# Performance work log

Hardware: AMD Instinct MI355X
Metric: run time of the kernel (lower is better)

## Reference

```python
import jax, jax.numpy as jnp
import numpy as np

N_NODES = 50000
N_EDGES = 1600000
N_FEAT = 128
HIDDEN = 128
N_GRAPHS = 64
N_CLASSES = 10
N_REGS = 1


def setup_inputs() -> dict:
    key = jax.random.key(0)
    ks = jax.random.split(key, 16)
    inp = {
        "x": jax.random.normal(ks[0], (N_NODES, N_FEAT), dtype=jnp.float32),
        "edge_index": jax.random.randint(ks[1], (2, N_EDGES), 0, N_NODES, dtype=jnp.int32),
        "batch": jnp.sort(jax.random.randint(ks[2], (N_NODES,), 0, N_GRAPHS, dtype=jnp.int32)),
        # GCNConv layer params (PyG: linear without bias applied first, bias added after aggregation)
        "w0": jax.random.normal(ks[3], (N_FEAT, HIDDEN), dtype=jnp.float32) * 0.05,
        "b0": jax.random.normal(ks[4], (HIDDEN,), dtype=jnp.float32) * 0.05,
        "w1": jax.random.normal(ks[5], (HIDDEN, HIDDEN), dtype=jnp.float32) * 0.05,
        "b1": jax.random.normal(ks[6], (HIDDEN,), dtype=jnp.float32) * 0.05,
        "w2": jax.random.normal(ks[7], (HIDDEN, HIDDEN), dtype=jnp.float32) * 0.05,
        "b2": jax.random.normal(ks[8], (HIDDEN,), dtype=jnp.float32) * 0.05,
        # heads
        "wc": jax.random.normal(ks[9], (HIDDEN, N_CLASSES), dtype=jnp.float32) * 0.05,
        "bc": jax.random.normal(ks[10], (N_CLASSES,), dtype=jnp.float32) * 0.05,
        "wr": jax.random.normal(ks[11], (HIDDEN, N_REGS), dtype=jnp.float32) * 0.05,
        "br": jax.random.normal(ks[12], (N_REGS,), dtype=jnp.float32) * 0.05,
    }
    return inp


def _gcn_layer(x, src, dst, w, b, deg_inv_sqrt, deg_inv):
    # x: [N, Din] -> [N, Dout]. GCNConv: D^-1/2 (A+I) D^-1/2 (x W) + b
    h = x @ w  # [N, Dout]
    coef = (deg_inv_sqrt[src] * deg_inv_sqrt[dst])[:, None]  # [E, 1]
    agg = jax.ops.segment_sum(h[src] * coef, dst, num_segments=x.shape[0])
    agg = agg + h * deg_inv[:, None]  # self-loop term: deg^-1 * h
    return agg + b


def reference(x, edge_index, batch, w0, b0, w1, b1, w2, b2, wc, bc, wr, br):
    src, dst = edge_index[0], edge_index[1]
    n = x.shape[0]
    # degrees include self-loop weight 1 (PyG gcn_norm with edge_weight=1)
    deg = jax.ops.segment_sum(jnp.ones(src.shape, x.dtype), dst, num_segments=n) + 1.0
    deg_inv_sqrt = deg ** -0.5
    deg_inv = 1.0 / deg

    h = _gcn_layer(x, src, dst, w0, b0, deg_inv_sqrt, deg_inv)
    h = _gcn_layer(jax.nn.elu(h), src, dst, w1, b1, deg_inv_sqrt, deg_inv)
    h = _gcn_layer(jax.nn.elu(h), src, dst, w2, b2, deg_inv_sqrt, deg_inv)

    # global mean pool over graphs
    sums = jax.ops.segment_sum(h, batch, num_segments=N_GRAPHS)  # [G, H]
    cnt = jax.ops.segment_sum(jnp.ones((n,), h.dtype), batch, num_segments=N_GRAPHS)
    pooled = sums / jnp.maximum(cnt, 1.0)[:, None]

    cls_out = pooled @ wc + bc
    reg_out = pooled @ wr + br
    return (pooled, cls_out, reg_out)
```

## Files before the change

kernel.cpp:

```cpp
#include <hip/hip_runtime.h>
#include <hip/hip_fp16.h>
#include <math.h>

#define N_NODES   50000
#define N_EDGES   1600000
#define NF        128
#define N_GRAPHS  64
#define N_CLASSES 10

#define NBK       391
#define BK_SHIFT  7
#define BK_NODES  128
#define SLAB      5120
#define CHUNK     4096
#define NCHUNKS   ((N_EDGES + CHUNK - 1) / CHUNK)

typedef _Float16 half8 __attribute__((ext_vector_type(8)));
typedef float f32x4 __attribute__((ext_vector_type(4)));

__global__ void k_zero(int* __restrict__ bucket_cur, float* __restrict__ sums) {
    int i = blockIdx.x * 256 + threadIdx.x;
    if (i < NBK) bucket_cur[i] = i * SLAB;
    if (i < N_GRAPHS * NF) sums[i] = 0.f;
}

__global__ __launch_bounds__(256) void k_bscatter(const int* __restrict__ src,
                                                  const int* __restrict__ dst,
                                                  int* __restrict__ bucket_cur,
                                                  int* __restrict__ pairs) {
    __shared__ int h[NBK], rb[NBK], c2[NBK];
    int t = threadIdx.x;
    for (int i = t; i < NBK; i += 256) { h[i] = 0; c2[i] = 0; }
    __syncthreads();
    int base = blockIdx.x * CHUNK;
    int end = min(base + CHUNK, N_EDGES);
    for (int e = base + t; e < end; e += 256)
        atomicAdd(&h[dst[e] >> BK_SHIFT], 1);
    __syncthreads();
    for (int i = t; i < NBK; i += 256)
        rb[i] = h[i] ? atomicAdd(&bucket_cur[i], h[i]) : 0;
    __syncthreads();
    for (int e = base + t; e < end; e += 256) {
        int d = dst[e];
        int b = d >> BK_SHIFT;
        int k = atomicAdd(&c2[b], 1);
        pairs[rb[b] + k] = (src[e] << BK_SHIFT) | (d & (BK_NODES - 1));
    }
}

__global__ __launch_bounds__(512) void k_bfill(const int* __restrict__ pairs,
                                               const int* __restrict__ bucket_cur,
                                               int* __restrict__ row_start,
                                               int* __restrict__ row_end,
                                               float* __restrict__ dis,
                                               int* __restrict__ csr_src) {
    __shared__ int cnt[BK_NODES];
    __shared__ int cur[BK_NODES];
    __shared__ int ts[512];
    int b = blockIdx.x, t = threadIdx.x;
    int node_base = b << BK_SHIFT;
    int lo = b * SLAB, hi = bucket_cur[b];

    if (t < BK_NODES) cnt[t] = 0;
    __syncthreads();
    for (int e = lo + t; e < hi; e += 512)
        atomicAdd(&cnt[pairs[e] & (BK_NODES - 1)], 1);
    __syncthreads();

    int a = (t < BK_NODES) ? cnt[t] : 0;
    ts[t] = a;
    __syncthreads();
    for (int off = 1; off < BK_NODES; off <<= 1) {
        int y = (t >= off) ? ts[t - off] : 0;
        __syncthreads();
        ts[t] += y;
        __syncthreads();
    }
    int row = lo + ts[t] - a;
    if (t < BK_NODES) {
        cur[t] = row;
        int n = node_base + t;
        if (n < N_NODES) {
            row_start[n] = row;
            row_end[n]   = row + a;
            dis[n] = rsqrtf((float)(a + 1));
        }
    }
    __syncthreads();

    for (int e = lo + t; e < hi; e += 512) {
        int p = pairs[e];
        int pos = atomicAdd(&cur[p & (BK_NODES - 1)], 1);
        csr_src[pos] = p >> BK_SHIFT;
    }
}

__global__ void k_xconv(const float* __restrict__ x, _Float16* __restrict__ xh) {
    int i = blockIdx.x * 256 + threadIdx.x;
    if (i >= N_NODES * NF / 4) return;
    float4 v = ((const float4*)x)[i];
    _Float16 h4[4] = {(_Float16)v.x, (_Float16)v.y, (_Float16)v.z, (_Float16)v.w};
    *(uint2*)&xh[(size_t)i * 4] = *(uint2*)h4;
}

__global__ void k_wconv(const float* __restrict__ w0, const float* __restrict__ w1,
                        const float* __restrict__ w2, _Float16* __restrict__ wf) {
    int b = blockIdx.x, t = threadIdx.x;
    const float* W = (b == 0) ? w0 : (b == 1) ? w1 : w2;
    _Float16* dst = wf + (size_t)b * NF * NF;
    for (int idx = t; idx < NF * NF; idx += 256) {
        int k = idx >> 7, n = idx & 127;
        int nt = n >> 4, kc = k >> 5, quad = (k >> 3) & 3, j = k & 7;
        int lane = quad * 16 + (n & 15);
        dst[((nt * 4 + kc) * 64 + lane) * 8 + j] = (_Float16)W[idx];
    }
}

template <bool ELU>
__global__ __launch_bounds__(256) void k_gemm(const _Float16* __restrict__ X,
                                              const _Float16* __restrict__ WF,
                                              const float* __restrict__ dis,
                                              __half* __restrict__ H) {
    __shared__ _Float16 xs[64 * 136];
    int t = threadIdx.x;
    int row0 = blockIdx.x * 64;
#pragma unroll
    for (int i = 0; i < 4; i++) {
        int f = i * 256 + t;
        int r = f >> 4, c = (f & 15) * 8;
        half8 v = {};
        int gr = row0 + r;
        if (gr < N_NODES) v = *(const half8*)&X[(size_t)gr * NF + c];
        if (ELU) {
#pragma unroll
            for (int j = 0; j < 8; j++) {
                float xv = (float)v[j];
                v[j] = (_Float16)(xv > 0.f ? xv : (expf(xv) - 1.f));
            }
        }
        *(half8*)&xs[r * 136 + c] = v;
    }
    __syncthreads();

    int w = t >> 6;
    int lane = t & 63;
    int m = lane & 15, quad = lane >> 4;

    half8 a[4];
#pragma unroll
    for (int kc = 0; kc < 4; kc++)
        a[kc] = *(const half8*)&xs[(w * 16 + m) * 136 + kc * 32 + quad * 8];

    f32x4 acc[8];
#pragma unroll
    for (int nt = 0; nt < 8; nt++) {
        f32x4 c4 = {0.f, 0.f, 0.f, 0.f};
#pragma unroll
        for (int kc = 0; kc < 4; kc++) {
            half8 bf = *(const half8*)&WF[((nt * 4 + kc) * 64 + lane) * 8];
            c4 = __builtin_amdgcn_mfma_f32_16x16x32_f16(a[kc], bf, c4, 0, 0, 0);
        }
        acc[nt] = c4;
    }

#pragma unroll
    for (int reg = 0; reg < 4; reg++) {
        int r = row0 + w * 16 + quad * 4 + reg;
        if (r < N_NODES) {
            float ds = dis[r];
#pragma unroll
            for (int nt = 0; nt < 8; nt++)
                H[(size_t)r * NF + nt * 16 + m] = __float2half(ds * acc[nt][reg]);
        }
    }
}

template <bool HALF_OUT>
__global__ __launch_bounds__(256) void k_agg(const __half* __restrict__ H,
                                             const float* __restrict__ bias,
                                             const int* __restrict__ row_start,
                                             const int* __restrict__ row_end,
                                             const int* __restrict__ csr_src,
                                             const float* __restrict__ dis,
                                             void* __restrict__ outv) {
    const uint2* H4 = (const uint2*)H;
    int wv   = (blockIdx.x * 256 + threadIdx.x) >> 6;
    int lane = threadIdx.x & 63;
    int node = wv * 2 + (lane >> 5);
    int l    = lane & 31;
    if (node >= N_NODES) return;
    int rs = row_start[node], re = row_end[node];
    float a0 = 0.f, a1 = 0.f, a2 = 0.f, a3 = 0.f;
    int e = rs;
    for (; e + 7 < re; e += 8) {
        uint2 v[8];
#pragma unroll
        for (int j = 0; j < 8; j++) {
            int s = csr_src[e + j];
            v[j] = H4[(size_t)s * 32 + l];
        }
#pragma unroll
        for (int j = 0; j < 8; j++) {
            float2 lo = __half22float2(*(__half2*)&v[j].x);
            float2 hi = __half22float2(*(__half2*)&v[j].y);
            a0 += lo.x; a1 += lo.y; a2 += hi.x; a3 += hi.y;
        }
    }
    for (; e < re; e++) {
        int s = csr_src[e];
        uint2 v = H4[(size_t)s * 32 + l];
        float2 lo = __half22float2(*(__half2*)&v.x);
        float2 hi = __half22float2(*(__half2*)&v.y);
        a0 += lo.x; a1 += lo.y; a2 += hi.x; a3 += hi.y;
    }
    {
        uint2 v = H4[(size_t)node * 32 + l];
        float2 lo = __half22float2(*(__half2*)&v.x);
        float2 hi = __half22float2(*(__half2*)&v.y);
        a0 += lo.x; a1 += lo.y; a2 += hi.x; a3 += hi.y;
    }
    float di = dis[node];
    int c = l * 4;
    float4 bv = *(const float4*)&bias[c];
    float o0 = a0 * di + bv.x, o1 = a1 * di + bv.y;
    float o2 = a2 * di + bv.z, o3 = a3 * di + bv.w;
    if (HALF_OUT) {
        uint2 o;
        *(__half2*)&o.x = __floats2half2_rn(o0, o1);
        *(__half2*)&o.y = __floats2half2_rn(o2, o3);
        ((uint2*)outv)[(size_t)node * 32 + l] = o;
    } else {
        *(float4*)&((float*)outv)[(size_t)node * NF + c] = make_float4(o0, o1, o2, o3);
    }
}

__global__ void k_pool(const float* __restrict__ A, const int* __restrict__ batch,
                       float* __restrict__ sums) {
    int b = blockIdx.x, t = threadIdx.x;
    int c = t & 127, th = t >> 7;
    int start = b * 256 + th;
    if (start >= N_NODES) return;
    int end = min(N_NODES, b * 256 + 256);
    float acc = 0.f;
    int gcur = batch[start];
    for (int i = start; i < end; i += 2) {
        int g = batch[i];
        if (g != gcur) {
            atomicAdd(&sums[gcur * NF + c], acc);
            acc = 0.f;
            gcur = g;
        }
        acc += A[(size_t)i * NF + c];
    }
    atomicAdd(&sums[gcur * NF + c], acc);
}

__global__ void k_head(const float* __restrict__ sums, const int* __restrict__ batch,
                       const float* __restrict__ wc, const float* __restrict__ bc,
                       const float* __restrict__ wr, const float* __restrict__ br,
                       float* __restrict__ out) {
    __shared__ float p[128];
    __shared__ int cnt_s;
    int g = blockIdx.x, c = threadIdx.x;
    if (c == 0) {
        int lo = 0, hi = N_NODES;
        while (lo < hi) { int m = (lo + hi) >> 1; if (batch[m] < g) lo = m + 1; else hi = m; }
        int s0 = lo;
        lo = 0; hi = N_NODES;
        while (lo < hi) { int m = (lo + hi) >> 1; if (batch[m] < g + 1) lo = m + 1; else hi = m; }
        cnt_s = lo - s0;
    }
    __syncthreads();
    float cnt = (float)max(cnt_s, 1);
    float pv = sums[g * NF + c] / cnt;
    p[c] = pv;
    out[g * NF + c] = pv;
    __syncthreads();
    if (c < N_CLASSES) {
        float d = bc[c];
        for (int k = 0; k < NF; k++) d += p[k] * wc[k * N_CLASSES + c];
        out[N_GRAPHS * NF + g * N_CLASSES + c] = d;
    }
    if (c == N_CLASSES) {
        float d = br[0];
        for (int k = 0; k < NF; k++) d += p[k] * wr[k];
        out[N_GRAPHS * NF + N_GRAPHS * N_CLASSES + g] = d;
    }
}

extern "C" void kernel_launch(void* const* d_in, const int* in_sizes, int n_in,
                              void* d_out, int out_size, void* d_ws, size_t ws_size,
                              hipStream_t stream) {
    const float* x     = (const float*)d_in[0];
    const int*   ei    = (const int*)d_in[1];
    const int*   batch = (const int*)d_in[2];
    const float* w0 = (const float*)d_in[3];
    const float* b0 = (const float*)d_in[4];
    const float* w1 = (const float*)d_in[5];
    const float* b1 = (const float*)d_in[6];
    const float* w2 = (const float*)d_in[7];
    const float* b2 = (const float*)d_in[8];
    const float* wc = (const float*)d_in[9];
    const float* bc = (const float*)d_in[10];
    const float* wr = (const float*)d_in[11];
    const float* br = (const float*)d_in[12];
    const int* srcp = ei;
    const int* dstp = ei + N_EDGES;
    float* out = (float*)d_out;

    char* ws = (char*)d_ws;
    size_t off = 0;
    auto alloc = [&](size_t bytes) -> void* {
        void* p = ws + off;
        off = (off + bytes + 255) & ~(size_t)255;
        return p;
    };
    const int NPAD = N_NODES + 64;
    int*      row_start  = (int*)alloc(N_NODES * 4);
    int*      row_end    = (int*)alloc(N_NODES * 4);
    int*      bucket_cur = (int*)alloc(NBK * 4);
    float*    dis        = (float*)alloc(N_NODES * 4);
    int*      csr_src    = (int*)alloc((size_t)NBK * SLAB * 4);
    __half*   Hbuf       = (__half*)alloc((size_t)NPAD * NF * 2);
    float*    Abuf       = (float*)alloc((size_t)NPAD * NF * 4);
    _Float16* xh         = (_Float16*)alloc((size_t)NPAD * NF * 2);
    _Float16* wf         = (_Float16*)alloc((size_t)3 * NF * NF * 2);
    float*    sums       = (float*)alloc(N_GRAPHS * NF * 4);
    (void)ws_size;
    int* pairs = (int*)Abuf;
    _Float16* Ah = xh;

    k_zero<<<32, 256, 0, stream>>>(bucket_cur, sums);
    k_bscatter<<<NCHUNKS, 256, 0, stream>>>(srcp, dstp, bucket_cur, pairs);
    k_bfill<<<NBK, 512, 0, stream>>>(pairs, bucket_cur, row_start, row_end, dis, csr_src);
    k_wconv<<<3, 256, 0, stream>>>(w0, w1, w2, wf);
    k_xconv<<<(N_NODES * NF / 4 + 255) / 256, 256, 0, stream>>>(x, xh);

    const int gemm_grid = (N_NODES + 63) / 64;
    const int agg_grid  = (N_NODES + 7) / 8;

    k_gemm<false><<<gemm_grid, 256, 0, stream>>>(xh, wf, dis, Hbuf);
    k_agg<true><<<agg_grid, 256, 0, stream>>>(Hbuf, b0, row_start, row_end, csr_src, dis, Ah);
    k_gemm<true><<<gemm_grid, 256, 0, stream>>>(Ah, wf + NF * NF, dis, Hbuf);
    k_agg<true><<<agg_grid, 256, 0, stream>>>(Hbuf, b1, row_start, row_end, csr_src, dis, Ah);
    k_gemm<true><<<gemm_grid, 256, 0, stream>>>(Ah, wf + 2 * NF * NF, dis, Hbuf);
    k_agg<false><<<agg_grid, 256, 0, stream>>>(Hbuf, b2, row_start, row_end, csr_src, dis, Abuf);

    k_pool<<<(N_NODES + 255) / 256, 256, 0, stream>>>(Abuf, batch, sums);
    k_head<<<N_GRAPHS, 128, 0, stream>>>(sums, batch, wc, bc, wr, br, out);
}
```

Baseline: 404.5 us.

## Fuse fp32 input conversion into GEMM, pooling into last aggregation, stage GEMM stores

The separate fp32-to-fp16 conversion kernel is removed, and the first GEMM now reads fp32 x directly and converts while loading into shared memory. The final aggregation now accumulates mean-pool sums through shared-memory atomics and global atomics, which removes the fp32 Abuf write and the separate pool kernel. GEMM output is staged through shared memory so it can be written with 16-byte vector stores instead of scattered 2-byte stores. In exchange, the last aggregation issues more atomics, and there are extra syncs in the GEMM.

```diff
diff --git a/kernel.cpp b/kernel.cpp
--- a/kernel.cpp
+++ b/kernel.cpp
@@ -95,14 +95,6 @@
     }
 }
 
-__global__ void k_xconv(const float* __restrict__ x, _Float16* __restrict__ xh) {
-    int i = blockIdx.x * 256 + threadIdx.x;
-    if (i >= N_NODES * NF / 4) return;
-    float4 v = ((const float4*)x)[i];
-    _Float16 h4[4] = {(_Float16)v.x, (_Float16)v.y, (_Float16)v.z, (_Float16)v.w};
-    *(uint2*)&xh[(size_t)i * 4] = *(uint2*)h4;
-}
-
 __global__ void k_wconv(const float* __restrict__ w0, const float* __restrict__ w1,
                         const float* __restrict__ w2, _Float16* __restrict__ wf) {
     int b = blockIdx.x, t = threadIdx.x;
@@ -116,21 +108,34 @@
     }
 }
 
-template <bool ELU>
-__global__ __launch_bounds__(256) void k_gemm(const _Float16* __restrict__ X,
+template <bool ELU, bool FP32IN>
+__global__ __launch_bounds__(256) void k_gemm(const void* __restrict__ Xv,
                                               const _Float16* __restrict__ WF,
                                               const float* __restrict__ dis,
                                               __half* __restrict__ H) {
     __shared__ _Float16 xs[64 * 136];
+    const _Float16* Xh = (const _Float16*)Xv;
+    const float*    Xf = (const float*)Xv;
     int t = threadIdx.x;
     int row0 = blockIdx.x * 64;
 #pragma unroll
     for (int i = 0; i < 4; i++) {
         int f = i * 256 + t;
         int r = f >> 4, c = (f & 15) * 8;
+        int gr = row0 + r;
         half8 v = {};
-        int gr = row0 + r;
-        if (gr < N_NODES) v = *(const half8*)&X[(size_t)gr * NF + c];
+        if (gr < N_NODES) {
+            if (FP32IN) {
+                float4 v0 = *(const float4*)&Xf[(size_t)gr * NF + c];
+                float4 v1 = *(const float4*)&Xf[(size_t)gr * NF + c + 4];
+                v[0] = (_Float16)v0.x; v[1] = (_Float16)v0.y;
+                v[2] = (_Float16)v0.z; v[3] = (_Float16)v0.w;
+                v[4] = (_Float16)v1.x; v[5] = (_Float16)v1.y;
+                v[6] = (_Float16)v1.z; v[7] = (_Float16)v1.w;
+            } else {
+                v = *(const half8*)&Xh[(size_t)gr * NF + c];
+            }
+        }
         if (ELU) {
 #pragma unroll
             for (int j = 0; j < 8; j++) {
@@ -163,96 +168,113 @@
         acc[nt] = c4;
     }
 
+    __syncthreads();
 #pragma unroll
     for (int reg = 0; reg < 4; reg++) {
-        int r = row0 + w * 16 + quad * 4 + reg;
-        if (r < N_NODES) {
-            float ds = dis[r];
-#pragma unroll
-            for (int nt = 0; nt < 8; nt++)
-                H[(size_t)r * NF + nt * 16 + m] = __float2half(ds * acc[nt][reg]);
-        }
-    }
-}
-
-template <bool HALF_OUT>
+        int r = w * 16 + quad * 4 + reg;
+        int gr = row0 + r;
+        float ds = (gr < N_NODES) ? dis[gr] : 0.f;
+#pragma unroll
+        for (int nt = 0; nt < 8; nt++)
+            xs[r * 136 + nt * 16 + m] = (_Float16)(ds * acc[nt][reg]);
+    }
+    __syncthreads();
+#pragma unroll
+    for (int i = 0; i < 4; i++) {
+        int f = i * 256 + t;
+        int r = f >> 4, c = (f & 15) * 8;
+        int gr = row0 + r;
+        if (gr < N_NODES)
+            *(half8*)&H[(size_t)gr * NF + c] = *(const half8*)&xs[r * 136 + c];
+    }
+}
+
+template <bool POOL>
 __global__ __launch_bounds__(256) void k_agg(const __half* __restrict__ H,
                                              const float* __restrict__ bias,
                                              const int* __restrict__ row_start,
                                              const int* __restrict__ row_end,
                                              const int* __restrict__ csr_src,
                                              const float* __restrict__ dis,
+                                             const int* __restrict__ batch,
                                              void* __restrict__ outv) {
+    __shared__ float pacc[NF];
     const uint2* H4 = (const uint2*)H;
-    int wv   = (blockIdx.x * 256 + threadIdx.x) >> 6;
-    int lane = threadIdx.x & 63;
-    int node = wv * 2 + (lane >> 5);
+    int t = threadIdx.x;
+    int lane = t & 63;
+    int node = blockIdx.x * 8 + (t >> 6) * 2 + (lane >> 5);
     int l    = lane & 31;
-    if (node >= N_NODES) return;
-    int rs = row_start[node], re = row_end[node];
-    float a0 = 0.f, a1 = 0.f, a2 = 0.f, a3 = 0.f;
-    int e = rs;
-    for (; e + 7 < re; e += 8) {
-        uint2 v[8];
-#pragma unroll
-        for (int j = 0; j < 8; j++) {
-            int s = csr_src[e + j];
-            v[j] = H4[(size_t)s * 32 + l];
-        }
-#pragma unroll
-        for (int j = 0; j < 8; j++) {
-            float2 lo = __half22float2(*(__half2*)&v[j].x);
-            float2 hi = __half22float2(*(__half2*)&v[j].y);
+    int c    = l * 4;
+    if (POOL) {
+        if (t < NF) pacc[t] = 0.f;
+        __syncthreads();
+    }
+    float o0 = 0.f, o1 = 0.f, o2 = 0.f, o3 = 0.f;
+    bool active = node < N_NODES;
+    if (active) {
+        int rs = row_start[node], re = row_end[node];
+        float a0 = 0.f, a1 = 0.f, a2 = 0.f, a3 = 0.f;
+        int e = rs;
+        for (; e + 7 < re; e += 8) {
+            uint2 v[8];
+#pragma unroll
+            for (int j = 0; j < 8; j++) {
+                int s = csr_src[e + j];
+                v[j] = H4[(size_t)s * 32 + l];
+            }
+#pragma unroll
+            for (int j = 0; j < 8; j++) {
+                float2 lo = __half22float2(*(__half2*)&v[j].x);
+                float2 hi = __half22float2(*(__half2*)&v[j].y);
+                a0 += lo.x; a1 += lo.y; a2 += hi.x; a3 += hi.y;
+            }
+        }
+        for (; e < re; e++) {
+            int s = csr_src[e];
+            uint2 v = H4[(size_t)s * 32 + l];
+            float2 lo = __half22float2(*(__half2*)&v.x);
+            float2 hi = __half22float2(*(__half2*)&v.y);
             a0 += lo.x; a1 += lo.y; a2 += hi.x; a3 += hi.y;
         }
-    }
-    for (; e < re; e++) {
-        int s = csr_src[e];
-        uint2 v = H4[(size_t)s * 32 + l];
-        float2 lo = __half22float2(*(__half2*)&v.x);
-        float2 hi = __half22float2(*(__half2*)&v.y);
-        a0 += lo.x; a1 += lo.y; a2 += hi.x; a3 += hi.y;
-    }
-    {
-        uint2 v = H4[(size_t)node * 32 + l];
-        float2 lo = __half22float2(*(__half2*)&v.x);
-        float2 hi = __half22float2(*(__half2*)&v.y);
-        a0 += lo.x; a1 += lo.y; a2 += hi.x; a3 += hi.y;
-    }
-    float di = dis[node];
-    int c = l * 4;
-    float4 bv = *(const float4*)&bias[c];
-    float o0 = a0 * di + bv.x, o1 = a1 * di + bv.y;
-    float o2 = a2 * di + bv.z, o3 = a3 * di + bv.w;
-    if (HALF_OUT) {
-        uint2 o;
-        *(__half2*)&o.x = __floats2half2_rn(o0, o1);
-        *(__half2*)&o.y = __floats2half2_rn(o2, o3);
-        ((uint2*)outv)[(size_t)node * 32 + l] = o;
-    } else {
-        *(float4*)&((float*)outv)[(size_t)node * NF + c] = make_float4(o0, o1, o2, o3);
-    }
-}
-
-__global__ void k_pool(const float* __restrict__ A, const int* __restrict__ batch,
-                       float* __restrict__ sums) {
-    int b = blockIdx.x, t = threadIdx.x;
-    int c = t & 127, th = t >> 7;
-    int start = b * 256 + th;
-    if (start >= N_NODES) return;
-    int end = min(N_NODES, b * 256 + 256);
-    float acc = 0.f;
-    int gcur = batch[start];
-    for (int i = start; i < end; i += 2) {
-        int g = batch[i];
-        if (g != gcur) {
-            atomicAdd(&sums[gcur * NF + c], acc);
-            acc = 0.f;
-            gcur = g;
-        }
-        acc += A[(size_t)i * NF + c];
-    }
-    atomicAdd(&sums[gcur * NF + c], acc);
+        {
+            uint2 v = H4[(size_t)node * 32 + l];
+            float2 lo = __half22float2(*(__half2*)&v.x);
+            float2 hi = __half22float2(*(__half2*)&v.y);
+            a0 += lo.x; a1 += lo.y; a2 += hi.x; a3 += hi.y;
+        }
+        float di = dis[node];
+        float4 bv = *(const float4*)&bias[c];
+        o0 = a0 * di + bv.x; o1 = a1 * di + bv.y;
+        o2 = a2 * di + bv.z; o3 = a3 * di + bv.w;
+        if (!POOL) {
+            uint2 o;
+            *(__half2*)&o.x = __floats2half2_rn(o0, o1);
+            *(__half2*)&o.y = __floats2half2_rn(o2, o3);
+            ((uint2*)outv)[(size_t)node * 32 + l] = o;
+        }
+    }
+    if (POOL) {
+        float* sums = (float*)outv;
+        int first = blockIdx.x * 8;
+        int last  = min(first + 7, N_NODES - 1);
+        int g0 = batch[first], g7 = batch[last];
+        if (active) {
+            if (g0 == g7) {
+                atomicAdd(&pacc[c + 0], o0);
+                atomicAdd(&pacc[c + 1], o1);
+                atomicAdd(&pacc[c + 2], o2);
+                atomicAdd(&pacc[c + 3], o3);
+            } else {
+                int g = batch[node];
+                atomicAdd(&sums[g * NF + c + 0], o0);
+                atomicAdd(&sums[g * NF + c + 1], o1);
+                atomicAdd(&sums[g * NF + c + 2], o2);
+                atomicAdd(&sums[g * NF + c + 3], o3);
+            }
+        }
+        __syncthreads();
+        if (t < NF && g0 == g7) atomicAdd(&sums[g0 * NF + t], pacc[t]);
+    }
 }
 
 __global__ void k_head(const float* __restrict__ sums, const int* __restrict__ batch,
@@ -315,37 +337,32 @@
         off = (off + bytes + 255) & ~(size_t)255;
         return p;
     };
-    const int NPAD = N_NODES + 64;
     int*      row_start  = (int*)alloc(N_NODES * 4);
     int*      row_end    = (int*)alloc(N_NODES * 4);
     int*      bucket_cur = (int*)alloc(NBK * 4);
     float*    dis        = (float*)alloc(N_NODES * 4);
     int*      csr_src    = (int*)alloc((size_t)NBK * SLAB * 4);
-    __half*   Hbuf       = (__half*)alloc((size_t)NPAD * NF * 2);
-    float*    Abuf       = (float*)alloc((size_t)NPAD * NF * 4);
-    _Float16* xh         = (_Float16*)alloc((size_t)NPAD * NF * 2);
+    __half*   Hbuf       = (__half*)alloc((size_t)N_NODES * NF * 2);
+    _Float16* Ah         = (_Float16*)alloc((size_t)N_NODES * NF * 2);
     _Float16* wf         = (_Float16*)alloc((size_t)3 * NF * NF * 2);
     float*    sums       = (float*)alloc(N_GRAPHS * NF * 4);
     (void)ws_size;
-    int* pairs = (int*)Abuf;
-    _Float16* Ah = xh;
+    int* pairs = (int*)Hbuf;
 
     k_zero<<<32, 256, 0, stream>>>(bucket_cur, sums);
     k_bscatter<<<NCHUNKS, 256, 0, stream>>>(srcp, dstp, bucket_cur, pairs);
     k_bfill<<<NBK, 512, 0, stream>>>(pairs, bucket_cur, row_start, row_end, dis, csr_src);
     k_wconv<<<3, 256, 0, stream>>>(w0, w1, w2, wf);
-    k_xconv<<<(N_NODES * NF / 4 + 255) / 256, 256, 0, stream>>>(x, xh);
 
     const int gemm_grid = (N_NODES + 63) / 64;
     const int agg_grid  = (N_NODES + 7) / 8;
 
-    k_gemm<false><<<gemm_grid, 256, 0, stream>>>(xh, wf, dis, Hbuf);
-    k_agg<true><<<agg_grid, 256, 0, stream>>>(Hbuf, b0, row_start, row_end, csr_src, dis, Ah);
-    k_gemm<true><<<gemm_grid, 256, 0, stream>>>(Ah, wf + NF * NF, dis, Hbuf);
-    k_agg<true><<<agg_grid, 256, 0, stream>>>(Hbuf, b1, row_start, row_end, csr_src, dis, Ah);
-    k_gemm<true><<<gemm_grid, 256, 0, stream>>>(Ah, wf + 2 * NF * NF, dis, Hbuf);
-    k_agg<false><<<agg_grid, 256, 0, stream>>>(Hbuf, b2, row_start, row_end, csr_src, dis, Abuf);
-
-    k_pool<<<(N_NODES + 255) / 256, 256, 0, stream>>>(Abuf, batch, sums);
+    k_gemm<false, true><<<gemm_grid, 256, 0, stream>>>(x, wf, dis, Hbuf);
+    k_agg<false><<<agg_grid, 256, 0, stream>>>(Hbuf, b0, row_start, row_end, csr_src, dis, batch, Ah);
+    k_gemm<true, false><<<gemm_grid, 256, 0, stream>>>(Ah, wf + NF * NF, dis, Hbuf);
+    k_agg<false><<<agg_grid, 256, 0, stream>>>(Hbuf, b1, row_start, row_end, csr_src, dis, batch, Ah);
+    k_gemm<true, false><<<gemm_grid, 256, 0, stream>>>(Ah, wf + 2 * NF * NF, dis, Hbuf);
+    k_agg<true><<<agg_grid, 256, 0, stream>>>(Hbuf, b2, row_start, row_end, csr_src, dis, batch, sums);
+
     k_head<<<N_GRAPHS, 128, 0, stream>>>(sums, batch, wc, bc, wr, br, out);
 }
```

Measured after the change: 375.7 us. -7.1%, faster.
